# Kernel optimization log

Measured on AMD Instinct MI355X. Metric: run time of the kernel, lower is better.

## Reference

```python
import jax, jax.numpy as jnp
import numpy as np

N, A, D, O = 8192, 32, 768, 256
LN_EPS = 1e-5


def setup_inputs() -> dict:
    key = jax.random.key(0)
    ks = jax.random.split(key, 9)
    articles = jax.random.normal(ks[0], (N, A, D), dtype=jnp.float32)
    counts = jax.random.randint(ks[1], (N,), 0, 33, dtype=jnp.int64)
    # Parameters (PyTorch Linear default-ish init scale)
    attn_w = jax.random.normal(ks[2], (D,), dtype=jnp.float32) / np.sqrt(D)
    attn_b = jax.random.normal(ks[3], (1,), dtype=jnp.float32) * 0.01
    proj_w = jax.random.normal(ks[4], (D, O), dtype=jnp.float32) / np.sqrt(D)
    proj_b = jax.random.normal(ks[5], (O,), dtype=jnp.float32) * 0.01
    ln_w = jnp.ones((O,), dtype=jnp.float32)
    ln_b = jnp.zeros((O,), dtype=jnp.float32)
    no_news = jax.random.normal(ks[6], (O,), dtype=jnp.float32) * 0.02
    return {"articles": articles, "counts": counts, "attn_w": attn_w,
            "attn_b": attn_b, "proj_w": proj_w, "proj_b": proj_b,
            "ln_w": ln_w, "ln_b": ln_b, "no_news": no_news}


def reference(articles, counts, attn_w, attn_b, proj_w, proj_b, ln_w, ln_b, no_news):
    # mask of valid (non-padded) articles: [N, A]
    mask = jnp.arange(A)[None, :] < counts[:, None]
    # attention scores per article: [N, A]
    scores = jnp.einsum('nad,d->na', articles, attn_w) + attn_b[0]
    scores = jnp.where(mask, scores, -1e9)
    # softmax over the (masked) article axis; count==1 reduces to weight 1,
    # matching the original squeeze(0) path exactly.
    weights = jax.nn.softmax(scores, axis=1)
    pooled = jnp.einsum('na,nad->nd', weights, articles)  # [N, D]
    # projection: Linear -> LayerNorm -> GELU (exact, erf-based as in torch)
    h = pooled @ proj_w + proj_b  # [N, O]
    mu = jnp.mean(h, axis=-1, keepdims=True)
    var = jnp.mean((h - mu) ** 2, axis=-1, keepdims=True)
    h_ln = (h - mu) / jnp.sqrt(var + LN_EPS) * ln_w + ln_b
    h_out = jax.nn.gelu(h_ln, approximate=False)
    # fallback to learned no-news embedding when there are zero articles
    return jnp.where(counts[:, None] > 0, h_out, no_news[None, :])
```

## Files before the change

### kernel.cpp

```cpp
#include <hip/hip_runtime.h>
#include <math.h>

#define N_ROWS 8192
#define A_ART  32
#define D_DIM  768
#define O_DIM  256
#define LN_EPS 1e-5f
#define R_TILE 16
#define P_STR  772

typedef unsigned short u16;
typedef unsigned int   u32;

__device__ __forceinline__ float bf2f(u16 u) { return __uint_as_float(((u32)u) << 16); }
__device__ __forceinline__ u16 f2bf(float f) {
    u32 x = __float_as_uint(f);
    return (u16)((x + 0x7fffu + ((x >> 16) & 1u)) >> 16);
}

#define WS_PROJW   256
#define WS_PARAMS  786688
#define WS_POOLED  793984
#define P_ATTNB    768
#define P_PROJB    800
#define P_LNW      1056
#define P_LNB      1312
#define P_NONEWS   1568

__global__ __launch_bounds__(64) void detect_kernel(const u32* __restrict__ art_w,
                                                    const int* __restrict__ cnt_w,
                                                    int* __restrict__ flags) {
    const int lane = threadIdx.x;
    u32 w = art_w[lane];
    u32 low = w & 0xffffu;
    u32 e = (low >> 7) & 0xffu;
    bool sane = (e >= 100u && e <= 140u) || ((low & 0x7fffu) == 0u);
    unsigned long long m1 = __ballot(sane);
    bool hz = true;
    if (lane < 32) hz = (cnt_w[2 * lane + 1] == 0);
    unsigned long long m2 = __ballot(hz);
    if (lane == 0) {
        flags[0] = (__popcll(m1) >= 48) ? 1 : 0;
        flags[1] = (m2 == ~0ull) ? 1 : 0;
    }
}

__device__ __forceinline__ float ldf(const void* p, int i, bool bf) {
    return bf ? bf2f(((const u16*)p)[i]) : ((const float*)p)[i];
}

__global__ __launch_bounds__(256) void params_kernel(const void* attn_w, const void* attn_b,
                                                     const void* proj_b, const void* ln_w,
                                                     const void* ln_b, const void* no_news,
                                                     const void* proj_w,
                                                     const int* __restrict__ flags,
                                                     float* __restrict__ projw_f,
                                                     float* __restrict__ params_f) {
    const bool bf = flags[0] != 0;
    const int b = blockIdx.x, t = threadIdx.x;
    if (b < 768) {
        int i = b * 256 + t;
        projw_f[i] = ldf(proj_w, i, bf);
    } else {
        int i = (b - 768) * 256 + t;
        if (i < 768)                    params_f[i] = ldf(attn_w, i, bf);
        else if (i == P_ATTNB)          params_f[i] = ldf(attn_b, 0, bf);
        else if (i >= P_PROJB  && i < P_PROJB  + 256) params_f[i] = ldf(proj_b,  i - P_PROJB,  bf);
        else if (i >= P_LNW    && i < P_LNW    + 256) params_f[i] = ldf(ln_w,    i - P_LNW,    bf);
        else if (i >= P_LNB    && i < P_LNB    + 256) params_f[i] = ldf(ln_b,    i - P_LNB,    bf);
        else if (i >= P_NONEWS && i < P_NONEWS + 256) params_f[i] = ldf(no_news, i - P_NONEWS, bf);
    }
}

#define ONLINE_STEP                                                          \
    {                                                                        \
        float s = 0.f;                                                       \
        _Pragma("unroll")                                                    \
        for (int k = 0; k < 12; ++k) s = fmaf(art[k], wfrag[k], s);          \
        _Pragma("unroll")                                                    \
        for (int off = 32; off; off >>= 1) s += __shfl_xor(s, off);          \
        s += bias;                                                           \
        float mn = fmaxf(m, s);                                              \
        float scale = __expf(m - mn);                                        \
        float p = __expf(s - mn);                                            \
        l = l * scale + p;                                                   \
        _Pragma("unroll")                                                    \
        for (int k = 0; k < 12; ++k) acc[k] = fmaf(p, art[k], acc[k] * scale); \
        m = mn;                                                              \
    }

__global__ __launch_bounds__(256) void pool_kernel(const void* __restrict__ articles,
                                                   const int* __restrict__ counts32,
                                                   const int* __restrict__ flags,
                                                   const float* __restrict__ params_f,
                                                   float* __restrict__ pooled) {
    __shared__ float lds_acc[4][D_DIM];
    __shared__ float lds_m[4];
    __shared__ float lds_l[4];

    const int n = blockIdx.x, t = threadIdx.x;
    const int wave = t >> 6, lane = t & 63;
    const int c = counts32[flags[1] ? 2 * n : n];

    if (c <= 0) {
        #pragma unroll
        for (int j = 0; j < 3; ++j) pooled[(size_t)n * D_DIM + t + 256 * j] = 0.0f;
        return;
    }

    float wfrag[12];
    #pragma unroll
    for (int j = 0; j < 3; ++j) {
        float4 wv = *(const float4*)(params_f + 4 * (lane + 64 * j));
        wfrag[4 * j + 0] = wv.x; wfrag[4 * j + 1] = wv.y;
        wfrag[4 * j + 2] = wv.z; wfrag[4 * j + 3] = wv.w;
    }
    const float bias = params_f[P_ATTNB];

    float m = -1e30f, l = 0.f;
    float acc[12];
    #pragma unroll
    for (int k = 0; k < 12; ++k) acc[k] = 0.f;

    if (flags[0]) {
        const u16* base = (const u16*)articles + (size_t)n * A_ART * D_DIM;
        for (int a = wave; a < c; a += 4) {
            float art[12];
            #pragma unroll
            for (int j = 0; j < 3; ++j) {
                uint2 q = *(const uint2*)(base + a * D_DIM + 4 * (lane + 64 * j));
                art[4 * j + 0] = bf2f((u16)(q.x & 0xffffu));
                art[4 * j + 1] = bf2f((u16)(q.x >> 16));
                art[4 * j + 2] = bf2f((u16)(q.y & 0xffffu));
                art[4 * j + 3] = bf2f((u16)(q.y >> 16));
            }
            ONLINE_STEP
        }
    } else {
        const float* base = (const float*)articles + (size_t)n * A_ART * D_DIM;
        for (int a = wave; a < c; a += 4) {
            float art[12];
            #pragma unroll
            for (int j = 0; j < 3; ++j) {
                float4 q = *(const float4*)(base + a * D_DIM + 4 * (lane + 64 * j));
                art[4 * j + 0] = q.x; art[4 * j + 1] = q.y;
                art[4 * j + 2] = q.z; art[4 * j + 3] = q.w;
            }
            ONLINE_STEP
        }
    }

    if (lane == 0) { lds_m[wave] = m; lds_l[wave] = l; }
    #pragma unroll
    for (int j = 0; j < 3; ++j) {
        *((float4*)&lds_acc[wave][4 * (lane + 64 * j)]) =
            make_float4(acc[4 * j + 0], acc[4 * j + 1], acc[4 * j + 2], acc[4 * j + 3]);
    }
    __syncthreads();

    float M = fmaxf(fmaxf(lds_m[0], lds_m[1]), fmaxf(lds_m[2], lds_m[3]));
    float e0 = __expf(lds_m[0] - M), e1 = __expf(lds_m[1] - M);
    float e2 = __expf(lds_m[2] - M), e3 = __expf(lds_m[3] - M);
    float L = lds_l[0] * e0 + lds_l[1] * e1 + lds_l[2] * e2 + lds_l[3] * e3;
    float invL = __frcp_rn(L);

    #pragma unroll
    for (int j = 0; j < 3; ++j) {
        const int d = t + 256 * j;
        float v = lds_acc[0][d] * e0 + lds_acc[1][d] * e1
                + lds_acc[2][d] * e2 + lds_acc[3][d] * e3;
        pooled[(size_t)n * D_DIM + d] = v * invL;
    }
}

__global__ __launch_bounds__(256) void proj_kernel(const float* __restrict__ pooled,
                                                   const float* __restrict__ projw_f,
                                                   const float* __restrict__ params_f,
                                                   const int* __restrict__ counts32,
                                                   const int* __restrict__ flags,
                                                   void* __restrict__ out) {
    __shared__ float lds_p[R_TILE * P_STR];
    __shared__ float lds_s[R_TILE * 16];
    __shared__ float lds_q[R_TILE * 16];
    __shared__ float lds_mu[R_TILE];
    __shared__ float lds_rs[R_TILE];

    const int t = threadIdx.x;
    const int row0 = blockIdx.x * R_TILE;
    const bool out_bf = flags[0] != 0;
    const bool c64 = flags[1] != 0;

    const float4* src = (const float4*)(pooled + (size_t)row0 * D_DIM);
    for (int q = t; q < R_TILE * (D_DIM / 4); q += 256) {
        int r  = q / (D_DIM / 4);
        int dc = (q % (D_DIM / 4)) * 4;
        *((float4*)&lds_p[r * P_STR + dc]) = src[q];
    }
    __syncthreads();

    const int r  = t & 15;
    const int ob = (t >> 4) * 16;

    float acc[16];
    #pragma unroll
    for (int j = 0; j < 16; ++j) acc[j] = 0.f;

    for (int d = 0; d < D_DIM; ++d) {
        const float pv = lds_p[r * P_STR + d];
        const float4* wrow = (const float4*)(projw_f + d * O_DIM + ob);
        float4 wa = wrow[0], wb = wrow[1], wc = wrow[2], wd = wrow[3];
        acc[0]  = fmaf(pv, wa.x, acc[0]);  acc[1]  = fmaf(pv, wa.y, acc[1]);
        acc[2]  = fmaf(pv, wa.z, acc[2]);  acc[3]  = fmaf(pv, wa.w, acc[3]);
        acc[4]  = fmaf(pv, wb.x, acc[4]);  acc[5]  = fmaf(pv, wb.y, acc[5]);
        acc[6]  = fmaf(pv, wb.z, acc[6]);  acc[7]  = fmaf(pv, wb.w, acc[7]);
        acc[8]  = fmaf(pv, wc.x, acc[8]);  acc[9]  = fmaf(pv, wc.y, acc[9]);
        acc[10] = fmaf(pv, wc.z, acc[10]); acc[11] = fmaf(pv, wc.w, acc[11]);
        acc[12] = fmaf(pv, wd.x, acc[12]); acc[13] = fmaf(pv, wd.y, acc[13]);
        acc[14] = fmaf(pv, wd.z, acc[14]); acc[15] = fmaf(pv, wd.w, acc[15]);
    }

    float ps = 0.f, pq = 0.f;
    #pragma unroll
    for (int j = 0; j < 16; ++j) {
        acc[j] += params_f[P_PROJB + ob + j];
        ps += acc[j];
        pq += acc[j] * acc[j];
    }
    lds_s[r * 16 + (t >> 4)] = ps;
    lds_q[r * 16 + (t >> 4)] = pq;
    __syncthreads();

    if (t < 16) {
        float s = 0.f, q = 0.f;
        #pragma unroll
        for (int g = 0; g < 16; ++g) { s += lds_s[t * 16 + g]; q += lds_q[t * 16 + g]; }
        float mu  = s * (1.0f / O_DIM);
        float var = q * (1.0f / O_DIM) - mu * mu;
        lds_mu[t] = mu;
        lds_rs[t] = rsqrtf(var + LN_EPS);
    }
    __syncthreads();

    const float mu = lds_mu[r];
    const float rs = lds_rs[r];
    const int row = row0 + r;
    const int cnt = counts32[c64 ? 2 * row : row];

    float vals[16];
    #pragma unroll
    for (int j = 0; j < 16; ++j) {
        const int o = ob + j;
        float x = (acc[j] - mu) * rs * params_f[P_LNW + o] + params_f[P_LNB + o];
        float g = 0.5f * x * (1.0f + erff(x * 0.70710678118654752f));
        vals[j] = (cnt > 0) ? g : params_f[P_NONEWS + o];
    }

    if (out_bf) {
        u16 obuf[16];
        #pragma unroll
        for (int j = 0; j < 16; ++j) obuf[j] = f2bf(vals[j]);
        uint4* dst = (uint4*)((u16*)out + (size_t)row * O_DIM + ob);
        dst[0] = *((const uint4*)&obuf[0]);
        dst[1] = *((const uint4*)&obuf[8]);
    } else {
        float4* dst = (float4*)((float*)out + (size_t)row * O_DIM + ob);
        dst[0] = *((const float4*)&vals[0]);
        dst[1] = *((const float4*)&vals[4]);
        dst[2] = *((const float4*)&vals[8]);
        dst[3] = *((const float4*)&vals[12]);
    }
}

extern "C" void kernel_launch(void* const* d_in, const int* in_sizes, int n_in,
                              void* d_out, int out_size, void* d_ws, size_t ws_size,
                              hipStream_t stream) {
    const void* articles = d_in[0];
    const int*  counts   = (const int*)d_in[1];

    int*   flags    = (int*)d_ws;
    float* projw_f  = (float*)((char*)d_ws + WS_PROJW);
    float* params_f = (float*)((char*)d_ws + WS_PARAMS);
    float* pooled   = (float*)((char*)d_ws + WS_POOLED);

    detect_kernel<<<1, 64, 0, stream>>>((const u32*)articles, counts, flags);
    params_kernel<<<776, 256, 0, stream>>>(d_in[2], d_in[3], d_in[5], d_in[6], d_in[7],
                                           d_in[8], d_in[4], flags, projw_f, params_f);
    pool_kernel<<<N_ROWS, 256, 0, stream>>>(articles, counts, flags, params_f, pooled);
    proj_kernel<<<N_ROWS / R_TILE, 256, 0, stream>>>(pooled, projw_f, params_f, counts,
                                                     flags, d_out);
}
```

Measured before the change: 1.146 ms.

## Fuse attention pooling and projection into one kernel, drop pooled round-trip

Merges the per-row softmax pooling kernel and the projection/LayerNorm/GELU kernel into one 512-thread kernel. Each wave pools two rows directly into shared memory, which removes the global write and re-read of the pooled intermediate and two extra launches. Dtype detection moves inside the kernels, and parameter conversion is skipped for fp32 inputs. In exchange, only 256 of 512 threads do the projection, each pooling wave walks all articles of a row serially, and there are only 512 blocks, which may lower memory-level parallelism on the article stream.

```diff
diff --git a/kernel.cpp b/kernel.cpp
--- a/kernel.cpp
+++ b/kernel.cpp
@@ -17,59 +17,29 @@
     u32 x = __float_as_uint(f);
     return (u16)((x + 0x7fffu + ((x >> 16) & 1u)) >> 16);
 }
-
-#define WS_PROJW   256
-#define WS_PARAMS  786688
-#define WS_POOLED  793984
-#define P_ATTNB    768
-#define P_PROJB    800
-#define P_LNW      1056
-#define P_LNB      1312
-#define P_NONEWS   1568
-
-__global__ __launch_bounds__(64) void detect_kernel(const u32* __restrict__ art_w,
-                                                    const int* __restrict__ cnt_w,
-                                                    int* __restrict__ flags) {
-    const int lane = threadIdx.x;
-    u32 w = art_w[lane];
-    u32 low = w & 0xffffu;
-    u32 e = (low >> 7) & 0xffu;
-    bool sane = (e >= 100u && e <= 140u) || ((low & 0x7fffu) == 0u);
-    unsigned long long m1 = __ballot(sane);
-    bool hz = true;
-    if (lane < 32) hz = (cnt_w[2 * lane + 1] == 0);
-    unsigned long long m2 = __ballot(hz);
-    if (lane == 0) {
-        flags[0] = (__popcll(m1) >= 48) ? 1 : 0;
-        flags[1] = (m2 == ~0ull) ? 1 : 0;
-    }
-}
-
 __device__ __forceinline__ float ldf(const void* p, int i, bool bf) {
     return bf ? bf2f(((const u16*)p)[i]) : ((const float*)p)[i];
 }
 
-__global__ __launch_bounds__(256) void params_kernel(const void* attn_w, const void* attn_b,
-                                                     const void* proj_b, const void* ln_w,
-                                                     const void* ln_b, const void* no_news,
-                                                     const void* proj_w,
-                                                     const int* __restrict__ flags,
-                                                     float* __restrict__ projw_f,
-                                                     float* __restrict__ params_f) {
-    const bool bf = flags[0] != 0;
-    const int b = blockIdx.x, t = threadIdx.x;
-    if (b < 768) {
-        int i = b * 256 + t;
-        projw_f[i] = ldf(proj_w, i, bf);
-    } else {
-        int i = (b - 768) * 256 + t;
-        if (i < 768)                    params_f[i] = ldf(attn_w, i, bf);
-        else if (i == P_ATTNB)          params_f[i] = ldf(attn_b, 0, bf);
-        else if (i >= P_PROJB  && i < P_PROJB  + 256) params_f[i] = ldf(proj_b,  i - P_PROJB,  bf);
-        else if (i >= P_LNW    && i < P_LNW    + 256) params_f[i] = ldf(ln_w,    i - P_LNW,    bf);
-        else if (i >= P_LNB    && i < P_LNB    + 256) params_f[i] = ldf(ln_b,    i - P_LNB,    bf);
-        else if (i >= P_NONEWS && i < P_NONEWS + 256) params_f[i] = ldf(no_news, i - P_NONEWS, bf);
-    }
+#define WS_PROJW 256
+
+__global__ __launch_bounds__(256) void convw_kernel(const void* __restrict__ proj_w,
+                                                    const u32* __restrict__ art_w,
+                                                    float* __restrict__ projw_f) {
+    __shared__ int sbf;
+    const int t = threadIdx.x;
+    if (t < 64) {
+        u32 w = art_w[t];
+        u32 low = w & 0xffffu;
+        u32 e = (low >> 7) & 0xffu;
+        bool sane = (e >= 100u && e <= 140u) || ((low & 0x7fffu) == 0u);
+        unsigned long long m1 = __ballot(sane);
+        if (t == 0) sbf = (__popcll(m1) >= 48) ? 1 : 0;
+    }
+    __syncthreads();
+    if (!sbf) return;
+    const int i = blockIdx.x * 256 + t;
+    projw_f[i] = bf2f(((const u16*)proj_w)[i]);
 }
 
 #define ONLINE_STEP                                                          \
@@ -89,185 +59,188 @@
         m = mn;                                                              \
     }
 
-__global__ __launch_bounds__(256) void pool_kernel(const void* __restrict__ articles,
-                                                   const int* __restrict__ counts32,
-                                                   const int* __restrict__ flags,
-                                                   const float* __restrict__ params_f,
-                                                   float* __restrict__ pooled) {
-    __shared__ float lds_acc[4][D_DIM];
-    __shared__ float lds_m[4];
-    __shared__ float lds_l[4];
-
-    const int n = blockIdx.x, t = threadIdx.x;
-    const int wave = t >> 6, lane = t & 63;
-    const int c = counts32[flags[1] ? 2 * n : n];
-
-    if (c <= 0) {
-        #pragma unroll
-        for (int j = 0; j < 3; ++j) pooled[(size_t)n * D_DIM + t + 256 * j] = 0.0f;
-        return;
-    }
-
-    float wfrag[12];
-    #pragma unroll
-    for (int j = 0; j < 3; ++j) {
-        float4 wv = *(const float4*)(params_f + 4 * (lane + 64 * j));
-        wfrag[4 * j + 0] = wv.x; wfrag[4 * j + 1] = wv.y;
-        wfrag[4 * j + 2] = wv.z; wfrag[4 * j + 3] = wv.w;
-    }
-    const float bias = params_f[P_ATTNB];
-
-    float m = -1e30f, l = 0.f;
-    float acc[12];
-    #pragma unroll
-    for (int k = 0; k < 12; ++k) acc[k] = 0.f;
-
-    if (flags[0]) {
-        const u16* base = (const u16*)articles + (size_t)n * A_ART * D_DIM;
-        for (int a = wave; a < c; a += 4) {
-            float art[12];
-            #pragma unroll
-            for (int j = 0; j < 3; ++j) {
-                uint2 q = *(const uint2*)(base + a * D_DIM + 4 * (lane + 64 * j));
-                art[4 * j + 0] = bf2f((u16)(q.x & 0xffffu));
-                art[4 * j + 1] = bf2f((u16)(q.x >> 16));
-                art[4 * j + 2] = bf2f((u16)(q.y & 0xffffu));
-                art[4 * j + 3] = bf2f((u16)(q.y >> 16));
-            }
-            ONLINE_STEP
-        }
-    } else {
-        const float* base = (const float*)articles + (size_t)n * A_ART * D_DIM;
-        for (int a = wave; a < c; a += 4) {
-            float art[12];
-            #pragma unroll
-            for (int j = 0; j < 3; ++j) {
-                float4 q = *(const float4*)(base + a * D_DIM + 4 * (lane + 64 * j));
-                art[4 * j + 0] = q.x; art[4 * j + 1] = q.y;
-                art[4 * j + 2] = q.z; art[4 * j + 3] = q.w;
-            }
-            ONLINE_STEP
-        }
-    }
-
-    if (lane == 0) { lds_m[wave] = m; lds_l[wave] = l; }
-    #pragma unroll
-    for (int j = 0; j < 3; ++j) {
-        *((float4*)&lds_acc[wave][4 * (lane + 64 * j)]) =
-            make_float4(acc[4 * j + 0], acc[4 * j + 1], acc[4 * j + 2], acc[4 * j + 3]);
-    }
-    __syncthreads();
-
-    float M = fmaxf(fmaxf(lds_m[0], lds_m[1]), fmaxf(lds_m[2], lds_m[3]));
-    float e0 = __expf(lds_m[0] - M), e1 = __expf(lds_m[1] - M);
-    float e2 = __expf(lds_m[2] - M), e3 = __expf(lds_m[3] - M);
-    float L = lds_l[0] * e0 + lds_l[1] * e1 + lds_l[2] * e2 + lds_l[3] * e3;
-    float invL = __frcp_rn(L);
-
-    #pragma unroll
-    for (int j = 0; j < 3; ++j) {
-        const int d = t + 256 * j;
-        float v = lds_acc[0][d] * e0 + lds_acc[1][d] * e1
-                + lds_acc[2][d] * e2 + lds_acc[3][d] * e3;
-        pooled[(size_t)n * D_DIM + d] = v * invL;
-    }
-}
-
-__global__ __launch_bounds__(256) void proj_kernel(const float* __restrict__ pooled,
-                                                   const float* __restrict__ projw_f,
-                                                   const float* __restrict__ params_f,
-                                                   const int* __restrict__ counts32,
-                                                   const int* __restrict__ flags,
-                                                   void* __restrict__ out) {
+__global__ __launch_bounds__(512, 4) void fused_kernel(
+        const void* __restrict__ articles, const int* __restrict__ counts32,
+        const void* __restrict__ attn_w, const void* __restrict__ attn_b,
+        const void* __restrict__ proj_b, const void* __restrict__ ln_w,
+        const void* __restrict__ ln_b, const void* __restrict__ no_news,
+        const float* __restrict__ projw_f, const void* __restrict__ proj_w_raw,
+        void* __restrict__ out) {
     __shared__ float lds_p[R_TILE * P_STR];
     __shared__ float lds_s[R_TILE * 16];
     __shared__ float lds_q[R_TILE * 16];
     __shared__ float lds_mu[R_TILE];
     __shared__ float lds_rs[R_TILE];
-
-    const int t = threadIdx.x;
+    __shared__ int   sflags[2];
+
+    const int t    = threadIdx.x;
+    const int wave = t >> 6, lane = t & 63;
+
+    if (t < 64) {
+        u32 w = ((const u32*)articles)[t];
+        u32 low = w & 0xffffu;
+        u32 e = (low >> 7) & 0xffu;
+        bool sane = (e >= 100u && e <= 140u) || ((low & 0x7fffu) == 0u);
+        unsigned long long m1 = __ballot(sane);
+        bool hz = true;
+        if (t < 32) hz = (counts32[2 * t + 1] == 0);
+        unsigned long long m2 = __ballot(hz);
+        if (t == 0) {
+            sflags[0] = (__popcll(m1) >= 48) ? 1 : 0;
+            sflags[1] = (m2 == ~0ull) ? 1 : 0;
+        }
+    }
+    __syncthreads();
+    const bool bf  = sflags[0] != 0;
+    const bool c64 = sflags[1] != 0;
+
+    float wfrag[12];
+    if (bf) {
+        const u16* aw = (const u16*)attn_w;
+        #pragma unroll
+        for (int j = 0; j < 3; ++j) {
+            uint2 q = *(const uint2*)(aw + 4 * (lane + 64 * j));
+            wfrag[4 * j + 0] = bf2f((u16)(q.x & 0xffffu));
+            wfrag[4 * j + 1] = bf2f((u16)(q.x >> 16));
+            wfrag[4 * j + 2] = bf2f((u16)(q.y & 0xffffu));
+            wfrag[4 * j + 3] = bf2f((u16)(q.y >> 16));
+        }
+    } else {
+        #pragma unroll
+        for (int j = 0; j < 3; ++j) {
+            float4 wv = *(const float4*)((const float*)attn_w + 4 * (lane + 64 * j));
+            wfrag[4 * j + 0] = wv.x; wfrag[4 * j + 1] = wv.y;
+            wfrag[4 * j + 2] = wv.z; wfrag[4 * j + 3] = wv.w;
+        }
+    }
+    const float bias = ldf(attn_b, 0, bf);
+
     const int row0 = blockIdx.x * R_TILE;
-    const bool out_bf = flags[0] != 0;
-    const bool c64 = flags[1] != 0;
-
-    const float4* src = (const float4*)(pooled + (size_t)row0 * D_DIM);
-    for (int q = t; q < R_TILE * (D_DIM / 4); q += 256) {
-        int r  = q / (D_DIM / 4);
-        int dc = (q % (D_DIM / 4)) * 4;
-        *((float4*)&lds_p[r * P_STR + dc]) = src[q];
-    }
-    __syncthreads();
-
-    const int r  = t & 15;
-    const int ob = (t >> 4) * 16;
+
+    for (int i = 0; i < 2; ++i) {
+        const int r = wave * 2 + i;
+        const int n = row0 + r;
+        const int c = counts32[c64 ? 2 * n : n];
+
+        float m = -1e30f, l = 0.f;
+        float acc[12];
+        #pragma unroll
+        for (int k = 0; k < 12; ++k) acc[k] = 0.f;
+
+        if (c > 0) {
+            if (bf) {
+                const u16* base = (const u16*)articles + (size_t)n * (A_ART * D_DIM);
+                for (int a = 0; a < c; ++a) {
+                    float art[12];
+                    #pragma unroll
+                    for (int j = 0; j < 3; ++j) {
+                        uint2 q = *(const uint2*)(base + a * D_DIM + 4 * (lane + 64 * j));
+                        art[4 * j + 0] = bf2f((u16)(q.x & 0xffffu));
+                        art[4 * j + 1] = bf2f((u16)(q.x >> 16));
+                        art[4 * j + 2] = bf2f((u16)(q.y & 0xffffu));
+                        art[4 * j + 3] = bf2f((u16)(q.y >> 16));
+                    }
+                    ONLINE_STEP
+                }
+            } else {
+                const float* base = (const float*)articles + (size_t)n * (A_ART * D_DIM);
+                for (int a = 0; a < c; ++a) {
+                    float art[12];
+                    #pragma unroll
+                    for (int j = 0; j < 3; ++j) {
+                        float4 q = *(const float4*)(base + a * D_DIM + 4 * (lane + 64 * j));
+                        art[4 * j + 0] = q.x; art[4 * j + 1] = q.y;
+                        art[4 * j + 2] = q.z; art[4 * j + 3] = q.w;
+                    }
+                    ONLINE_STEP
+                }
+            }
+            const float invL = __frcp_rn(l);
+            #pragma unroll
+            for (int k = 0; k < 12; ++k) acc[k] *= invL;
+        }
+        #pragma unroll
+        for (int j = 0; j < 3; ++j)
+            *((float4*)&lds_p[r * P_STR + 4 * (lane + 64 * j)]) =
+                make_float4(acc[4 * j + 0], acc[4 * j + 1], acc[4 * j + 2], acc[4 * j + 3]);
+    }
+    __syncthreads();
+
+    const bool active = (t < 256);
+    const int  tr = t & 15;
+    const int  ob = (t >> 4) * 16;
 
     float acc[16];
     #pragma unroll
     for (int j = 0; j < 16; ++j) acc[j] = 0.f;
 
-    for (int d = 0; d < D_DIM; ++d) {
-        const float pv = lds_p[r * P_STR + d];
-        const float4* wrow = (const float4*)(projw_f + d * O_DIM + ob);
-        float4 wa = wrow[0], wb = wrow[1], wc = wrow[2], wd = wrow[3];
-        acc[0]  = fmaf(pv, wa.x, acc[0]);  acc[1]  = fmaf(pv, wa.y, acc[1]);
-        acc[2]  = fmaf(pv, wa.z, acc[2]);  acc[3]  = fmaf(pv, wa.w, acc[3]);
-        acc[4]  = fmaf(pv, wb.x, acc[4]);  acc[5]  = fmaf(pv, wb.y, acc[5]);
-        acc[6]  = fmaf(pv, wb.z, acc[6]);  acc[7]  = fmaf(pv, wb.w, acc[7]);
-        acc[8]  = fmaf(pv, wc.x, acc[8]);  acc[9]  = fmaf(pv, wc.y, acc[9]);
-        acc[10] = fmaf(pv, wc.z, acc[10]); acc[11] = fmaf(pv, wc.w, acc[11]);
-        acc[12] = fmaf(pv, wd.x, acc[12]); acc[13] = fmaf(pv, wd.y, acc[13]);
-        acc[14] = fmaf(pv, wd.z, acc[14]); acc[15] = fmaf(pv, wd.w, acc[15]);
-    }
-
-    float ps = 0.f, pq = 0.f;
-    #pragma unroll
-    for (int j = 0; j < 16; ++j) {
-        acc[j] += params_f[P_PROJB + ob + j];
-        ps += acc[j];
-        pq += acc[j] * acc[j];
-    }
-    lds_s[r * 16 + (t >> 4)] = ps;
-    lds_q[r * 16 + (t >> 4)] = pq;
+    if (active) {
+        const float* W = bf ? projw_f : (const float*)proj_w_raw;
+        for (int d = 0; d < D_DIM; ++d) {
+            const float pv = lds_p[tr * P_STR + d];
+            const float4* wrow = (const float4*)(W + d * O_DIM + ob);
+            float4 wa = wrow[0], wb = wrow[1], wc = wrow[2], wd = wrow[3];
+            acc[0]  = fmaf(pv, wa.x, acc[0]);  acc[1]  = fmaf(pv, wa.y, acc[1]);
+            acc[2]  = fmaf(pv, wa.z, acc[2]);  acc[3]  = fmaf(pv, wa.w, acc[3]);
+            acc[4]  = fmaf(pv, wb.x, acc[4]);  acc[5]  = fmaf(pv, wb.y, acc[5]);
+            acc[6]  = fmaf(pv, wb.z, acc[6]);  acc[7]  = fmaf(pv, wb.w, acc[7]);
+            acc[8]  = fmaf(pv, wc.x, acc[8]);  acc[9]  = fmaf(pv, wc.y, acc[9]);
+            acc[10] = fmaf(pv, wc.z, acc[10]); acc[11] = fmaf(pv, wc.w, acc[11]);
+            acc[12] = fmaf(pv, wd.x, acc[12]); acc[13] = fmaf(pv, wd.y, acc[13]);
+            acc[14] = fmaf(pv, wd.z, acc[14]); acc[15] = fmaf(pv, wd.w, acc[15]);
+        }
+        float ps = 0.f, pq = 0.f;
+        #pragma unroll
+        for (int j = 0; j < 16; ++j) {
+            acc[j] += ldf(proj_b, ob + j, bf);
+            ps += acc[j];
+            pq += acc[j] * acc[j];
+        }
+        lds_s[tr * 16 + (t >> 4)] = ps;
+        lds_q[tr * 16 + (t >> 4)] = pq;
+    }
     __syncthreads();
 
     if (t < 16) {
-        float s = 0.f, q = 0.f;
-        #pragma unroll
-        for (int g = 0; g < 16; ++g) { s += lds_s[t * 16 + g]; q += lds_q[t * 16 + g]; }
+        float s = 0.f, qq = 0.f;
+        #pragma unroll
+        for (int g = 0; g < 16; ++g) { s += lds_s[t * 16 + g]; qq += lds_q[t * 16 + g]; }
         float mu  = s * (1.0f / O_DIM);
-        float var = q * (1.0f / O_DIM) - mu * mu;
+        float var = qq * (1.0f / O_DIM) - mu * mu;
         lds_mu[t] = mu;
         lds_rs[t] = rsqrtf(var + LN_EPS);
     }
     __syncthreads();
 
-    const float mu = lds_mu[r];
-    const float rs = lds_rs[r];
-    const int row = row0 + r;
-    const int cnt = counts32[c64 ? 2 * row : row];
-
-    float vals[16];
-    #pragma unroll
-    for (int j = 0; j < 16; ++j) {
-        const int o = ob + j;
-        float x = (acc[j] - mu) * rs * params_f[P_LNW + o] + params_f[P_LNB + o];
-        float g = 0.5f * x * (1.0f + erff(x * 0.70710678118654752f));
-        vals[j] = (cnt > 0) ? g : params_f[P_NONEWS + o];
-    }
-
-    if (out_bf) {
-        u16 obuf[16];
-        #pragma unroll
-        for (int j = 0; j < 16; ++j) obuf[j] = f2bf(vals[j]);
-        uint4* dst = (uint4*)((u16*)out + (size_t)row * O_DIM + ob);
-        dst[0] = *((const uint4*)&obuf[0]);
-        dst[1] = *((const uint4*)&obuf[8]);
-    } else {
-        float4* dst = (float4*)((float*)out + (size_t)row * O_DIM + ob);
-        dst[0] = *((const float4*)&vals[0]);
-        dst[1] = *((const float4*)&vals[4]);
-        dst[2] = *((const float4*)&vals[8]);
-        dst[3] = *((const float4*)&vals[12]);
+    if (active) {
+        const float mu = lds_mu[tr];
+        const float rs = lds_rs[tr];
+        const int row = row0 + tr;
+        const int cnt = counts32[c64 ? 2 * row : row];
+
+        float vals[16];
+        #pragma unroll
+        for (int j = 0; j < 16; ++j) {
+            const int o = ob + j;
+            float x = (acc[j] - mu) * rs * ldf(ln_w, o, bf) + ldf(ln_b, o, bf);
+            float g = 0.5f * x * (1.0f + erff(x * 0.70710678118654752f));
+            vals[j] = (cnt > 0) ? g : ldf(no_news, o, bf);
+        }
+
+        if (bf) {
+            u16 obuf[16];
+            #pragma unroll
+            for (int j = 0; j < 16; ++j) obuf[j] = f2bf(vals[j]);
+            uint4* dst = (uint4*)((u16*)out + (size_t)row * O_DIM + ob);
+            dst[0] = *((const uint4*)&obuf[0]);
+            dst[1] = *((const uint4*)&obuf[8]);
+        } else {
+            float4* dst = (float4*)((float*)out + (size_t)row * O_DIM + ob);
+            dst[0] = *((const float4*)&vals[0]);
+            dst[1] = *((const float4*)&vals[4]);
+            dst[2] = *((const float4*)&vals[8]);
+            dst[3] = *((const float4*)&vals[12]);
+        }
     }
 }
 
@@ -276,16 +249,10 @@
                               hipStream_t stream) {
     const void* articles = d_in[0];
     const int*  counts   = (const int*)d_in[1];
-
-    int*   flags    = (int*)d_ws;
-    float* projw_f  = (float*)((char*)d_ws + WS_PROJW);
-    float* params_f = (float*)((char*)d_ws + WS_PARAMS);
-    float* pooled   = (float*)((char*)d_ws + WS_POOLED);
-
-    detect_kernel<<<1, 64, 0, stream>>>((const u32*)articles, counts, flags);
-    params_kernel<<<776, 256, 0, stream>>>(d_in[2], d_in[3], d_in[5], d_in[6], d_in[7],
-                                           d_in[8], d_in[4], flags, projw_f, params_f);
-    pool_kernel<<<N_ROWS, 256, 0, stream>>>(articles, counts, flags, params_f, pooled);
-    proj_kernel<<<N_ROWS / R_TILE, 256, 0, stream>>>(pooled, projw_f, params_f, counts,
-                                                     flags, d_out);
-}
+    float* projw_f = (float*)((char*)d_ws + WS_PROJW);
+
+    convw_kernel<<<768, 256, 0, stream>>>(d_in[4], (const u32*)articles, projw_f);
+    fused_kernel<<<N_ROWS / R_TILE, 512, 0, stream>>>(
+        articles, counts, d_in[2], d_in[3], d_in[5], d_in[6], d_in[7], d_in[8],
+        projw_f, d_in[4], d_out);
+}
```

Measured after the change: 1.140 ms. No clear change (-0.6%).
